# Performance work log

Hardware: AMD Instinct MI355X
Metric: run time of the kernel (lower is better)

## Reference

```python
import jax, jax.numpy as jnp
import numpy as np

B, T, D, H = 4, 4096, 1024, 16
HD = D // H

def _phi(x):
    # ELU + 1 feature map (positive values)
    return jax.nn.elu(x) + 1.0

def setup_inputs() -> dict:
    key = jax.random.key(0)
    ks = jax.random.split(key, 6)
    s = D ** -0.5
    return {
        "x": jax.random.normal(ks[0], (B, T, D), dtype=jnp.float32),
        "mask": jax.random.randint(ks[1], (B, 1, 1, T), 0, 2).astype(bool),
        "Wq": jax.random.normal(ks[2], (D, D), dtype=jnp.float32) * s,
        "Wk": jax.random.normal(ks[3], (D, D), dtype=jnp.float32) * s,
        "Wv": jax.random.normal(ks[4], (D, D), dtype=jnp.float32) * s,
        "Wo": jax.random.normal(ks[5], (D, D), dtype=jnp.float32) * s,
    }

def reference(x, mask, Wq, Wk, Wv, Wo):
    b, t, d = x.shape
    def proj(W):
        # nn.Linear: y = x @ W.T ; split heads -> (B, H, T, HD)
        return (x @ W.T).reshape(b, t, H, HD).transpose(0, 2, 1, 3)
    q = _phi(proj(Wq))
    k = _phi(proj(Wk))
    v = proj(Wv)
    # mask.transpose(-2,-1): (B,1,1,T) -> (B,1,T,1); True positions zeroed
    m = jnp.swapaxes(mask, -2, -1)
    k = jnp.where(m, 0.0, k)
    v = jnp.where(m, 0.0, v)
    # kv = k^T v : (B,H,HD,HD) global pooling over T
    kv = jnp.einsum('bhtd,bhte->bhde', k, v)
    k_sum = k.sum(axis=-2)  # (B,H,HD)
    out = jnp.einsum('bhtd,bhde->bhte', q, kv)  # (B,H,T,HD)
    norm = jnp.maximum(jnp.einsum('bhtd,bhd->bht', q, k_sum)[..., None], 1e-6)
    out = (out / norm).transpose(0, 2, 1, 3).reshape(b, t, d)
    return out @ Wo.T  # dropout=0 (eval) -> identity
```

## Files before the change

kernel.cpp:

```cpp
#include <hip/hip_runtime.h>
#include <hip/hip_bf16.h>
#include <stdint.h>

#define T_ 4096
#define M_ 16384

typedef __attribute__((ext_vector_type(8))) short short8;
typedef __attribute__((ext_vector_type(4))) float f32x4;

__device__ __forceinline__ short f2b(float f) {
    __hip_bfloat16 h = __float2bfloat16(f);
    return __builtin_bit_cast(short, h);
}
__device__ __forceinline__ float b2f(short s) {
    unsigned int u = ((unsigned int)(unsigned short)s) << 16;
    return __builtin_bit_cast(float, u);
}
__device__ __forceinline__ void gload16(const void* g, void* l) {
    __builtin_amdgcn_global_load_lds(
        (const __attribute__((address_space(1))) void*)(unsigned long long)(uintptr_t)g,
        (__attribute__((address_space(3))) void*)(unsigned int)(uintptr_t)l,
        16, 0, 0);
}

__global__ __launch_bounds__(256) void cvt_x(const float* __restrict__ in,
                                             short* __restrict__ out) {
    long i = ((long)blockIdx.x * 256 + threadIdx.x) * 4;
    float4 f = *(const float4*)(in + i);
    short4 o; o.x = f2b(f.x); o.y = f2b(f.y); o.z = f2b(f.z); o.w = f2b(f.w);
    *(short4*)(out + i) = o;
}

__global__ __launch_bounds__(256) void cvt_weights(
    const float* __restrict__ Wq, const float* __restrict__ Wk,
    const float* __restrict__ Wv, const float* __restrict__ Wo,
    short* __restrict__ wqkvb, short* __restrict__ wob) {
    long i = ((long)blockIdx.x * 256 + threadIdx.x) * 4;
    int region = (int)(i >> 20);
    long off = i & 1048575;
    const float* src = region == 0 ? Wq : region == 1 ? Wk : region == 2 ? Wv : Wo;
    short* dst = region < 3 ? wqkvb + (long)region * 1048576 : wob;
    float4 f = *(const float4*)(src + off);
    short4 o; o.x = f2b(f.x); o.y = f2b(f.y); o.z = f2b(f.z); o.w = f2b(f.w);
    *(short4*)(dst + off) = o;
}

template <int MODE>
__global__ __launch_bounds__(512) void gemm4s(
    const short* __restrict__ A, const short* __restrict__ Bw,
    const int* __restrict__ mask,
    short* __restrict__ oQ, short* __restrict__ oK, short* __restrict__ oV,
    float* __restrict__ oF) {
    extern __shared__ short lds[];
    const int tid = threadIdx.x;
    const int wave = tid >> 6, lane = tid & 63;
    const int wm = wave >> 2, wn = wave & 3;

    const int nwg = gridDim.x;
    const int cpx = nwg >> 3;
    const int wg = (blockIdx.x & 7) * cpx + (blockIdx.x >> 3);
    const int bm = wg & 63, bn = wg >> 6;
    const long m0 = (long)bm * 256, n0 = (long)bn * 256;

    f32x4 acc[8][4];
#pragma unroll
    for (int i = 0; i < 8; ++i)
#pragma unroll
        for (int j = 0; j < 4; ++j) acc[i][j] = (f32x4)(0.0f);

    const short* aStageBase = A + (m0 + (lane >> 3)) * 1024 +
                              (((lane & 7) ^ (lane >> 3)) * 8);
    const short* bStageBase = Bw + (n0 + (lane >> 3)) * 1024 +
                              (((lane & 7) ^ (lane >> 3)) * 8);

    auto stageA = [&](int t) {
        const int d = t & 1;
#pragma unroll
        for (int j = 0; j < 4; ++j) {
            const int r = wave * 8 + j * 64;
            gload16(aStageBase + (long)r * 1024 + t * 64, lds + d * 16384 + r * 64);
        }
    };
    auto stageB = [&](int t) {
        const int d = t & 1;
#pragma unroll
        for (int j = 0; j < 4; ++j) {
            const int r = wave * 8 + j * 64;
            gload16(bStageBase + (long)r * 1024 + t * 64,
                    lds + 32768 + d * 16384 + r * 64);
        }
    };

    const int laneR = lane & 15;
    const int sBase = (((lane >> 4) ^ (lane & 7)) * 8);

    short8 alo[4][2], ahi[4][2], blo[2][2], bhi[2][2];
    auto rdAlo = [&](int d) {
#pragma unroll
        for (int m = 0; m < 4; ++m)
#pragma unroll
            for (int kk = 0; kk < 2; ++kk)
                alo[m][kk] = *(const short8*)(lds + d * 16384 + wm * 8192 +
                                              (m * 16 + laneR) * 64 +
                                              (sBase ^ (kk * 32)));
    };
    auto rdAhi = [&](int d) {
#pragma unroll
        for (int m = 0; m < 4; ++m)
#pragma unroll
            for (int kk = 0; kk < 2; ++kk)
                ahi[m][kk] = *(const short8*)(lds + d * 16384 + wm * 8192 +
                                              ((m + 4) * 16 + laneR) * 64 +
                                              (sBase ^ (kk * 32)));
    };
    auto rdBlo = [&](int d) {
#pragma unroll
        for (int n = 0; n < 2; ++n)
#pragma unroll
            for (int kk = 0; kk < 2; ++kk)
                blo[n][kk] = *(const short8*)(lds + 32768 + d * 16384 +
                                              (wn >> 1) * 8192 +
                                              ((wn & 1) * 64 + n * 16 + laneR) * 64 +
                                              (sBase ^ (kk * 32)));
    };
    auto rdBhi = [&](int d) {
#pragma unroll
        for (int n = 0; n < 2; ++n)
#pragma unroll
            for (int kk = 0; kk < 2; ++kk)
                bhi[n][kk] = *(const short8*)(lds + 32768 + d * 16384 +
                                              (wn >> 1) * 8192 +
                                              ((wn & 1) * 64 + (n + 2) * 16 + laneR) * 64 +
                                              (sBase ^ (kk * 32)));
    };
    auto mm = [&](short8 (&a)[4][2], short8 (&b)[2][2], int mo, int no) {
        __builtin_amdgcn_s_setprio(1);
#pragma unroll
        for (int m = 0; m < 4; ++m)
#pragma unroll
            for (int n = 0; n < 2; ++n)
#pragma unroll
                for (int kk = 0; kk < 2; ++kk)
                    acc[mo + m][no + n] = __builtin_amdgcn_mfma_f32_16x16x32_bf16(
                        a[m][kk], b[n][kk], acc[mo + m][no + n], 0, 0, 0);
        __builtin_amdgcn_s_setprio(0);
    };

#define BAR()    __builtin_amdgcn_s_barrier()
#define LGKM0()  asm volatile("s_waitcnt lgkmcnt(0)" ::: "memory")
#define VMW0()   asm volatile("s_waitcnt vmcnt(0)" ::: "memory")
#define SCHED0() __builtin_amdgcn_sched_barrier(0)

    stageA(0); stageB(0);
    VMW0();
    BAR();
    SCHED0();

    for (int t = 0; t < 16; ++t) {
        const int d = t & 1;
        if (t + 1 < 16) stageA(t + 1);
        rdAlo(d); rdBlo(d);
        BAR(); LGKM0(); SCHED0();
        mm(alo, blo, 0, 0);
        BAR(); SCHED0();
        if (t + 1 < 16) stageB(t + 1);
        rdAhi(d);
        BAR(); LGKM0(); SCHED0();
        mm(ahi, blo, 4, 0);
        BAR(); SCHED0();
        rdBhi(d);
        BAR(); LGKM0(); SCHED0();
        mm(ahi, bhi, 4, 2);
        BAR(); SCHED0();
        mm(alo, bhi, 0, 2);
        VMW0();
        BAR(); SCHED0();
    }

    if (MODE == 0) {
        const int sec = (int)(n0 >> 10);
        short* outp = sec == 0 ? oQ : (sec == 1 ? oK : oV);
        const long cbase = n0 & 1023;
#pragma unroll
        for (int mi = 0; mi < 8; ++mi) {
#pragma unroll
            for (int r = 0; r < 4; ++r) {
                long gm = m0 + wm * 128 + mi * 16 + (lane >> 4) * 4 + r;
                int mz = (sec >= 1) ? mask[gm] : 0;
#pragma unroll
                for (int ni = 0; ni < 4; ++ni) {
                    long gn = cbase + wn * 64 + ni * 16 + (lane & 15);
                    float v = acc[mi][ni][r];
                    if (sec <= 1) v = (v > 0.f) ? v + 1.f : __expf(v);
                    if (mz) v = 0.f;
                    outp[gm * 1024 + gn] = f2b(v);
                }
            }
        }
    } else {
#pragma unroll
        for (int mi = 0; mi < 8; ++mi)
#pragma unroll
            for (int r = 0; r < 4; ++r) {
                long gm = m0 + wm * 128 + mi * 16 + (lane >> 4) * 4 + r;
#pragma unroll
                for (int ni = 0; ni < 4; ++ni) {
                    long gn = n0 + wn * 64 + ni * 16 + (lane & 15);
                    oF[gm * 1024 + gn] = acc[mi][ni][r];
                }
            }
    }
#undef BAR
#undef LGKM0
#undef VMW0
#undef SCHED0
}

__global__ __launch_bounds__(256) void kv_partial(
    const short* __restrict__ Kb, const short* __restrict__ Vb,
    float* __restrict__ kvp, float* __restrict__ ksp) {
    __shared__ __align__(16) float Ks[64][64];
    __shared__ __align__(16) float Vs[64][64];
    const int c = blockIdx.x, bh = blockIdx.y;
    const int b = bh >> 4, h = bh & 15;
    const int tid = threadIdx.x;
    const int dk = tid & 63, g = tid >> 6;
    float acc[16];
#pragma unroll
    for (int j = 0; j < 16; ++j) acc[j] = 0.f;
    float ks = 0.f;
    const long rowbase = (long)b * T_ + (long)c * 256;
    const int col0 = h * 64;

    for (int s = 0; s < 4; ++s) {
        __syncthreads();
        {
            int rr = tid >> 2;
            int cc = (tid & 3) * 16;
            const long gr = rowbase + s * 64 + rr;
            const short* kp = Kb + gr * 1024 + col0 + cc;
            const short* vp = Vb + gr * 1024 + col0 + cc;
            short8 k0 = *(const short8*)(kp);
            short8 k1 = *(const short8*)(kp + 8);
            short8 v0 = *(const short8*)(vp);
            short8 v1 = *(const short8*)(vp + 8);
            float kf[16], vf[16];
#pragma unroll
            for (int e = 0; e < 8; ++e) {
                kf[e] = b2f(k0[e]); kf[8 + e] = b2f(k1[e]);
                vf[e] = b2f(v0[e]); vf[8 + e] = b2f(v1[e]);
            }
#pragma unroll
            for (int q = 0; q < 4; ++q) {
                *(f32x4*)&Ks[rr][cc + q * 4] = *(f32x4*)&kf[q * 4];
                *(f32x4*)&Vs[rr][cc + q * 4] = *(f32x4*)&vf[q * 4];
            }
        }
        __syncthreads();
#pragma unroll 8
        for (int tt = 0; tt < 64; ++tt) {
            float kv_ = Ks[tt][dk];
            if (g == 0) ks += kv_;
            f32x4 v0 = *(const f32x4*)&Vs[tt][g * 16];
            f32x4 v1 = *(const f32x4*)&Vs[tt][g * 16 + 4];
            f32x4 v2 = *(const f32x4*)&Vs[tt][g * 16 + 8];
            f32x4 v3 = *(const f32x4*)&Vs[tt][g * 16 + 12];
#pragma unroll
            for (int e = 0; e < 4; ++e) {
                acc[e] += kv_ * v0[e];  acc[4 + e] += kv_ * v1[e];
                acc[8 + e] += kv_ * v2[e]; acc[12 + e] += kv_ * v3[e];
            }
        }
    }
    float* dst = kvp + ((long)bh * 16 + c) * 4096 + dk * 64 + g * 16;
#pragma unroll
    for (int q = 0; q < 4; ++q) *(f32x4*)(dst + q * 4) = *(f32x4*)&acc[q * 4];
    if (g == 0) ksp[((long)bh * 16 + c) * 64 + dk] = ks;
}

__global__ __launch_bounds__(256) void kv_reduce(
    const float* __restrict__ kvp, const float* __restrict__ ksp,
    short* __restrict__ kvT) {
    const int bh = blockIdx.x;
    const int tid = threadIdx.x;
    for (int e = tid; e < 4096; e += 256) {
        int dk = e >> 6, dv = e & 63;
        float s = 0.f;
#pragma unroll
        for (int c = 0; c < 16; ++c) s += kvp[((long)bh * 16 + c) * 4096 + e];
        kvT[(long)bh * 5120 + dv * 64 + dk] = f2b(s);
    }
    if (tid < 64) {
        float s = 0.f;
#pragma unroll
        for (int c = 0; c < 16; ++c) s += ksp[((long)bh * 16 + c) * 64 + tid];
        kvT[(long)bh * 5120 + 64 * 64 + tid] = f2b(s);
    }
    for (int e = tid; e < 15 * 64; e += 256)
        kvT[(long)bh * 5120 + 65 * 64 + e] = 0;
}

__global__ __launch_bounds__(256) void attn_out(
    const short* __restrict__ Qb, const short* __restrict__ kvT,
    short* __restrict__ attn) {
    __shared__ __align__(16) short Qs[128 * 64];
    const int tb = blockIdx.x, bh = blockIdx.y;
    const int b = bh >> 4, h = bh & 15;
    const int tid = threadIdx.x, wave = tid >> 6, lane = tid & 63;
    const long trow0 = (long)b * T_ + (long)tb * 128;
    const int col0 = h * 64;

    const int lr = lane >> 3, lc = (lane & 7) * 8;
    const short* qsrc = Qb + (trow0 + wave * 8 + lr) * 1024 + col0 + lc;
#pragma unroll
    for (int is = 0; is < 4; ++is)
        gload16(qsrc + (long)is * 32 * 1024, Qs + is * 2048 + wave * 512);

    short8 bfr[5][2];
    const short* kvb = kvT + (long)bh * 5120;
#pragma unroll
    for (int nf = 0; nf < 5; ++nf)
#pragma unroll
        for (int kk = 0; kk < 2; ++kk)
            bfr[nf][kk] = *(const short8*)(kvb + (nf * 16 + (lane & 15)) * 64 +
                                           kk * 32 + (lane >> 4) * 8);
    __syncthreads();

#pragma unroll
    for (int tf = 0; tf < 2; ++tf) {
        short8 af[2];
        int ar = wave * 32 + tf * 16 + (lane & 15);
#pragma unroll
        for (int kk = 0; kk < 2; ++kk)
            af[kk] = *(const short8*)(Qs + ar * 64 + kk * 32 + (lane >> 4) * 8);
        f32x4 oacc[5];
#pragma unroll
        for (int nf = 0; nf < 5; ++nf) {
            oacc[nf] = (f32x4)(0.0f);
#pragma unroll
            for (int kk = 0; kk < 2; ++kk)
                oacc[nf] = __builtin_amdgcn_mfma_f32_16x16x32_bf16(
                    af[kk], bfr[nf][kk], oacc[nf], 0, 0, 0);
        }
#pragma unroll
        for (int r = 0; r < 4; ++r) {
            float nv = __shfl(oacc[4][r], lane & 48, 64);
            nv = fmaxf(nv, 1e-6f);
            long gm = trow0 + wave * 32 + tf * 16 + (lane >> 4) * 4 + r;
#pragma unroll
            for (int nf = 0; nf < 4; ++nf) {
                float v = oacc[nf][r] / nv;
                attn[gm * 1024 + col0 + nf * 16 + (lane & 15)] = f2b(v);
            }
        }
    }
}

extern "C" void kernel_launch(void* const* d_in, const int* in_sizes, int n_in,
                              void* d_out, int out_size, void* d_ws, size_t ws_size,
                              hipStream_t stream) {
    const float* x = (const float*)d_in[0];
    const int* mask = (const int*)d_in[1];
    const float* Wq = (const float*)d_in[2];
    const float* Wk = (const float*)d_in[3];
    const float* Wv = (const float*)d_in[4];
    const float* Wo = (const float*)d_in[5];
    float* out = (float*)d_out;
    char* ws = (char*)d_ws;

    short* xb    = (short*)(ws);
    short* wqkvb = (short*)(ws + 33554432);
    short* wob   = (short*)(ws + 39845888);
    short* Qb    = (short*)(ws + 41943040);
    short* Kb    = (short*)(ws + 75497472);
    short* Vb    = (short*)(ws + 109051904);
    float* kvp   = (float*)(ws + 142606336);
    float* ksp   = (float*)(ws + 159383552);
    short* kvT   = (short*)(ws + 159645696);
    short* attnb = xb;

    hipFuncSetAttribute((const void*)gemm4s<0>,
                        hipFuncAttributeMaxDynamicSharedMemorySize, 131072);
    hipFuncSetAttribute((const void*)gemm4s<1>,
                        hipFuncAttributeMaxDynamicSharedMemorySize, 131072);

    cvt_x<<<16384, 256, 0, stream>>>(x, xb);
    cvt_weights<<<4096, 256, 0, stream>>>(Wq, Wk, Wv, Wo, wqkvb, wob);
    gemm4s<0><<<768, 512, 131072, stream>>>(xb, wqkvb, mask, Qb, Kb, Vb, nullptr);
    kv_partial<<<dim3(16, 64), 256, 0, stream>>>(Kb, Vb, kvp, ksp);
    kv_reduce<<<64, 256, 0, stream>>>(kvp, ksp, kvT);
    attn_out<<<dim3(32, 64), 256, 0, stream>>>(Qb, kvT, attnb);
    gemm4s<1><<<256, 512, 131072, stream>>>(attnb, wob, nullptr, nullptr, nullptr,
                                            nullptr, out);
}
```

Before: 258.1 us.

## Restructure GEMM main loop into finer-grained software pipeline with partial waits

Reworks the bf16 GEMM k-loop so global-to-LDS staging is split into half-tile chunks issued further ahead, and LDS fragment reads for the next iteration are prefetched during the current MFMA phases. Full vmcnt/lgkmcnt(0) waits are replaced with counted partial waits so memory traffic overlaps with matrix math. This aims to hide load latency in both projection GEMMs, at the cost of more complex barrier and wait-count reasoning that could introduce races if counts are wrong.

```diff
diff --git a/kernel.cpp b/kernel.cpp
--- a/kernel.cpp
+++ b/kernel.cpp
@@ -46,7 +46,7 @@
 }
 
 template <int MODE>
-__global__ __launch_bounds__(512) void gemm4s(
+__global__ __launch_bounds__(512) void gemm8r(
     const short* __restrict__ A, const short* __restrict__ Bw,
     const int* __restrict__ mask,
     short* __restrict__ oQ, short* __restrict__ oK, short* __restrict__ oV,
@@ -73,19 +73,12 @@
     const short* bStageBase = Bw + (n0 + (lane >> 3)) * 1024 +
                               (((lane & 7) ^ (lane >> 3)) * 8);
 
-    auto stageA = [&](int t) {
+    auto stageAB = [&](int t, int h) {
         const int d = t & 1;
 #pragma unroll
-        for (int j = 0; j < 4; ++j) {
-            const int r = wave * 8 + j * 64;
+        for (int j = 0; j < 2; ++j) {
+            const int r = h * 128 + wave * 8 + j * 64;
             gload16(aStageBase + (long)r * 1024 + t * 64, lds + d * 16384 + r * 64);
-        }
-    };
-    auto stageB = [&](int t) {
-        const int d = t & 1;
-#pragma unroll
-        for (int j = 0; j < 4; ++j) {
-            const int r = wave * 8 + j * 64;
             gload16(bStageBase + (long)r * 1024 + t * 64,
                     lds + 32768 + d * 16384 + r * 64);
         }
@@ -147,34 +140,46 @@
     };
 
 #define BAR()    __builtin_amdgcn_s_barrier()
-#define LGKM0()  asm volatile("s_waitcnt lgkmcnt(0)" ::: "memory")
-#define VMW0()   asm volatile("s_waitcnt vmcnt(0)" ::: "memory")
+#define LGKM(n)  asm volatile("s_waitcnt lgkmcnt(" #n ")" ::: "memory")
+#define VMW(n)   asm volatile("s_waitcnt vmcnt(" #n ")" ::: "memory")
 #define SCHED0() __builtin_amdgcn_sched_barrier(0)
 
-    stageA(0); stageB(0);
-    VMW0();
+    stageAB(0, 0);
+    stageAB(0, 1);
+    VMW(0);
     BAR();
     SCHED0();
+    stageAB(1, 0);
+    rdAlo(0); rdBhi(0); rdBlo(0);
 
     for (int t = 0; t < 16; ++t) {
-        const int d = t & 1;
-        if (t + 1 < 16) stageA(t + 1);
-        rdAlo(d); rdBlo(d);
-        BAR(); LGKM0(); SCHED0();
+        const int d = t & 1, dn = d ^ 1;
+        if (t + 1 < 16) stageAB(t + 1, 1);
+        rdAhi(d);
+        BAR();
+        LGKM(8);
+        SCHED0();
         mm(alo, blo, 0, 0);
-        BAR(); SCHED0();
-        if (t + 1 < 16) stageB(t + 1);
-        rdAhi(d);
-        BAR(); LGKM0(); SCHED0();
+        BAR();
+        mm(alo, bhi, 0, 2);
+        LGKM(0);
+        VMW(2);
+        BAR();
+        SCHED0();
+        if (t + 1 < 16) rdAlo(dn);
+        if (t + 2 < 16) stageAB(t + 2, 0);
+        BAR();
+        if (t == 15) { LGKM(0); } else { LGKM(8); }
+        SCHED0();
+        mm(ahi, bhi, 4, 2);
+        if (t + 2 < 16) { VMW(4); } else { VMW(0); }
+        BAR();
+        SCHED0();
+        if (t + 1 < 16) rdBhi(dn);
+        BAR();
         mm(ahi, blo, 4, 0);
-        BAR(); SCHED0();
-        rdBhi(d);
-        BAR(); LGKM0(); SCHED0();
-        mm(ahi, bhi, 4, 2);
-        BAR(); SCHED0();
-        mm(alo, bhi, 0, 2);
-        VMW0();
-        BAR(); SCHED0();
+        if (t + 1 < 16) rdBlo(dn);
+        BAR();
     }
 
     if (MODE == 0) {
@@ -211,8 +216,8 @@
             }
     }
 #undef BAR
-#undef LGKM0
-#undef VMW0
+#undef LGKM
+#undef VMW
 #undef SCHED0
 }
 
@@ -379,17 +384,17 @@
     short* kvT   = (short*)(ws + 159645696);
     short* attnb = xb;
 
-    hipFuncSetAttribute((const void*)gemm4s<0>,
+    hipFuncSetAttribute((const void*)gemm8r<0>,
                         hipFuncAttributeMaxDynamicSharedMemorySize, 131072);
-    hipFuncSetAttribute((const void*)gemm4s<1>,
+    hipFuncSetAttribute((const void*)gemm8r<1>,
                         hipFuncAttributeMaxDynamicSharedMemorySize, 131072);
 
     cvt_x<<<16384, 256, 0, stream>>>(x, xb);
     cvt_weights<<<4096, 256, 0, stream>>>(Wq, Wk, Wv, Wo, wqkvb, wob);
-    gemm4s<0><<<768, 512, 131072, stream>>>(xb, wqkvb, mask, Qb, Kb, Vb, nullptr);
+    gemm8r<0><<<768, 512, 131072, stream>>>(xb, wqkvb, mask, Qb, Kb, Vb, nullptr);
     kv_partial<<<dim3(16, 64), 256, 0, stream>>>(Kb, Vb, kvp, ksp);
     kv_reduce<<<64, 256, 0, stream>>>(kvp, ksp, kvT);
     attn_out<<<dim3(32, 64), 256, 0, stream>>>(Qb, kvT, attnb);
-    gemm4s<1><<<256, 512, 131072, stream>>>(attnb, wob, nullptr, nullptr, nullptr,
+    gemm8r<1><<<256, 512, 131072, stream>>>(attnb, wob, nullptr, nullptr, nullptr,
                                             nullptr, out);
 }
```

Measured after the change: 260.7 us. No clear change (+1.0%).
